# Kernel tuning notes

Hardware: AMD Instinct MI355X
Metric: run time of the kernel (lower is better)

Reference implementation:

```python
import jax, jax.numpy as jnp
import numpy as np


def setup_inputs() -> dict:
    key = jax.random.key(0)
    ks = jax.random.split(key, 9)
    bs, F, T, d_in, Nh, d_out = 4, 8, 256, 64, 8, 64
    std = 2.0  # gaussian_init_delta_std
    return {
        "X": jax.random.normal(ks[0], (bs, F, T, d_in), dtype=jnp.float32),
        "attention_center": std * jax.random.normal(ks[1], (F, Nh, 1), dtype=jnp.float32),
        "alpha": jax.random.normal(ks[2], (F,), dtype=jnp.float32),
        "W_query": jax.random.normal(ks[3], (F, T, d_in, Nh, 2), dtype=jnp.float32),
        "W_key": jax.random.normal(ks[4], (F, T, d_in, Nh, 2), dtype=jnp.float32),
        "Wkey_": jax.random.normal(ks[5], (F, 2, 2), dtype=jnp.float32),
        "u": jax.random.normal(ks[6], (F, T, 2), dtype=jnp.float32),
        "W": jax.random.normal(ks[7], (F, Nh * d_in, d_out), dtype=jnp.float32),
        "b": jax.random.normal(ks[8], (F, T, d_out), dtype=jnp.float32),
    }


def reference(X, attention_center, alpha, W_query, W_key, Wkey_, u, W, b):
    bs, F, T, d_in = X.shape
    Nh = W_query.shape[3]

    # relative-position features R[t,l] = (l-t)^2, (l-t); identical across F in the original
    rel = (jnp.arange(T)[None, :] - jnp.arange(T)[:, None]).astype(jnp.float32)
    R = jnp.stack([rel ** 2, rel], axis=-1)  # (T,T,2)

    query = jnp.einsum('bftd,ftdhe->bfthe', X, W_query)  # (bs,F,T,Nh,2)
    key = jnp.einsum('bftd,ftdhe->bfthe', X, W_key)      # (bs,F,T,Nh,2)

    r_delta = jnp.einsum('fde,tle->ftld', Wkey_, R)      # (F,T,T,2)

    centers = jnp.concatenate([jnp.ones_like(attention_center), -2.0 * attention_center], axis=-1)  # (F,Nh,2)
    v = -alpha[:, None, None] * centers                  # (F,Nh,2)

    scores = (
        jnp.einsum('bfthe,bflhe->bfthl', query, key)
        + jnp.einsum('bfthe,ftle->bfthl', query, r_delta)
        + jnp.einsum('fle,bfthe->bfthl', u, key)
        + jnp.einsum('fhe,ftle->fthl', v, r_delta)[None]
    )  # (bs,F,T,Nh,T)

    probs = jax.nn.softmax(scores, axis=-1)

    vals = jnp.einsum('bfthl,bfld->bfthd', probs, X)     # (bs,F,T,Nh,d_in)
    vals = vals.reshape(bs, F, T, Nh * d_in)

    return jnp.einsum('bftd,fdo->bfto', vals, W) + b     # (bs,F,T,d_out)
```

## Files before the change

### kernel.cpp

```cpp
#include <hip/hip_runtime.h>
#include <hip/hip_bf16.h>

#define BS 4
#define NF 8
#define NT 256
#define DIN 64
#define NH 8
#define DOUT 64
#define TT 8
#define MROWS 64
#define NCHUNK 32

typedef unsigned short u16;
typedef __attribute__((ext_vector_type(8))) short short8;
typedef __attribute__((ext_vector_type(4))) float f32x4;
typedef __attribute__((ext_vector_type(4))) unsigned int u32x4;

static __device__ __forceinline__ u16 f2bf(float x) {
    __hip_bfloat16 h = __float2bfloat16(x);
    u16 r; __builtin_memcpy(&r, &h, 2); return r;
}
static __device__ __forceinline__ unsigned pk2(float a, float b) {
    return (unsigned)f2bf(a) | ((unsigned)f2bf(b) << 16);
}

__global__ __launch_bounds__(256) void prep_kernel(
    const float* __restrict__ X,
    const float* __restrict__ Wq,
    const float* __restrict__ Wk,
    const float* __restrict__ W,
    float* __restrict__ q,
    float* __restrict__ k,
    u16* __restrict__ XT,
    u16* __restrict__ Wt)
{
    __shared__ float sT[64][65];
    const int tid = threadIdx.x;
    const int bid = blockIdx.x;

    if (bid < 1024) {
        const int gw = (bid << 2) + (tid >> 6);
        const int which = gw >> 11;
        const int ft = gw & 2047;
        const int f = ft >> 8, t = ft & 255;
        const int ln = tid & 63;
        const int dg = ln >> 4;
        const int b  = (ln >> 2) & 3;
        const int hq = ln & 3;

        const float* wmat = which ? Wk : Wq;
        const float* wp = wmat + ((size_t)ft << 10) + (dg << 8) + (hq << 2);
        const float* xp = X + (((size_t)((b * NF + f) * NT + t)) << 6) + (dg << 4);

        float4 acc = {0.f, 0.f, 0.f, 0.f};
        #pragma unroll
        for (int j = 0; j < 16; ++j) {
            float xv = xp[j];
            float4 w4 = *(const float4*)(wp + (j << 4));
            acc.x = fmaf(xv, w4.x, acc.x);
            acc.y = fmaf(xv, w4.y, acc.y);
            acc.z = fmaf(xv, w4.z, acc.z);
            acc.w = fmaf(xv, w4.w, acc.w);
        }
        #pragma unroll
        for (int off = 16; off <= 32; off <<= 1) {
            acc.x += __shfl_xor(acc.x, off);
            acc.y += __shfl_xor(acc.y, off);
            acc.z += __shfl_xor(acc.z, off);
            acc.w += __shfl_xor(acc.w, off);
        }
        if (dg == 0) {
            float* outp = which ? k : q;
            *(float4*)(outp + (((size_t)((b * NF + f) * NT + t)) << 4) + (hq << 2)) = acc;
        }
    } else if (bid < 1056) {
        const int bf = bid - 1024;
        for (int lc = 0; lc < 4; ++lc) {
            #pragma unroll
            for (int i = 0; i < 16; ++i) {
                int l = i * 4 + (tid >> 6), d = tid & 63;
                sT[l][d] = X[(((size_t)(bf * NT) + lc * 64 + l) << 6) + d];
            }
            __syncthreads();
            #pragma unroll
            for (int i = 0; i < 16; ++i) {
                int d = i * 4 + (tid >> 6), l = tid & 63;
                XT[(((size_t)(bf * 64) + d) << 8) + lc * 64 + l] = f2bf(sT[l][d]);
            }
            __syncthreads();
        }
    } else {
        const int idx = bid - 1056;
        const int f = idx >> 3, kc = idx & 7;
        #pragma unroll
        for (int i = 0; i < 16; ++i) {
            int kk = i * 4 + (tid >> 6), o = tid & 63;
            sT[kk][o] = W[(((size_t)(f * 512) + kc * 64 + kk) << 6) + o];
        }
        __syncthreads();
        #pragma unroll
        for (int i = 0; i < 16; ++i) {
            int o = i * 4 + (tid >> 6), kk = tid & 63;
            Wt[(((size_t)(f * 64) + o) << 9) + kc * 64 + kk] = f2bf(sT[kk][o]);
        }
    }
}

__global__ __launch_bounds__(256, 3) void attn_kernel(
    const float* __restrict__ ac,
    const float* __restrict__ alpha,
    const float* __restrict__ Wkey_,
    const float* __restrict__ u,
    const float* __restrict__ bias,
    const float* __restrict__ q,
    const float* __restrict__ kws,
    const u16* __restrict__ XT,
    const u16* __restrict__ Wt,
    float* __restrict__ out)
{
    __shared__ u16  sP[MROWS * 256];
    __shared__ float sKU[4608];
    __shared__ float sRed[8 * MROWS];
    __shared__ float sM[MROWS];
    __shared__ float sInvS[MROWS];

    const int tid = threadIdx.x;
    const int bid = blockIdx.x;
    const int ch = bid & 31;
    const int f  = (bid >> 5) & 7;
    const int b  = bid >> 8;
    const int bf = b * NF + f;
    const int t0 = ch * TT;

    {
        const float4* k4 = (const float4*)(kws + ((size_t)bf << 12));
        float4* d4 = (float4*)sKU;
        #pragma unroll
        for (int i = 0; i < 4; ++i) d4[i * 256 + tid] = k4[i * 256 + tid];
        if (tid < 128) ((float4*)(sKU + 4096))[tid] = ((const float4*)(u + f * 512))[tid];
    }
    __syncthreads();

    const int h  = tid & 7;
    const int tp = (tid >> 3) & 3;
    const int le = tid >> 5;
    const int t_a = t0 + tp * 2, t_b = t_a + 1;
    const int m_a = tp * 16 + h, m_b = m_a + 8;
    const int lbase = le * 32;

    float q0a, q1a, kt0a, kt1a, c2a, c1a;
    float q0b, q1b, kt0b, kt1b, c2b, c1b;
    {
        float al = alpha[f];
        float acv = ac[f * 8 + h];
        float wk0 = Wkey_[f * 4],     wk1 = Wkey_[f * 4 + 1];
        float wk2 = Wkey_[f * 4 + 2], wk3 = Wkey_[f * 4 + 3];
        float2 qa = *(const float2*)(q + ((size_t)(bf * NT + t_a) << 4) + (h << 1));
        float2 qb = *(const float2*)(q + ((size_t)(bf * NT + t_b) << 4) + (h << 1));
        q0a = qa.x; q1a = qa.y; q0b = qb.x; q1b = qb.y;
        kt0a = sKU[t_a * 16 + h * 2]; kt1a = sKU[t_a * 16 + h * 2 + 1];
        kt0b = sKU[t_b * 16 + h * 2]; kt1b = sKU[t_b * 16 + h * 2 + 1];
        float a0 = q0a - al, a1 = q1a + 2.f * al * acv;
        c2a = a0 * wk0 + a1 * wk2; c1a = a0 * wk1 + a1 * wk3;
        a0 = q0b - al; a1 = q1b + 2.f * al * acv;
        c2b = a0 * wk0 + a1 * wk2; c1b = a0 * wk1 + a1 * wk3;
    }

    float mxa = -1e30f, mxb = -1e30f;
    {
        float rela = (float)(lbase - t_a);
        #pragma unroll 8
        for (int j = 0; j < 32; ++j) {
            int l = lbase + j;
            float2 K = *(const float2*)(sKU + l * 16 + h * 2);
            float2 U = *(const float2*)(sKU + 4096 + l * 2);
            float relb = rela - 1.f;
            float sa = (c2a * rela + c1a) * rela;
            sa = fmaf(q0a, K.x, sa); sa = fmaf(q1a, K.y, sa);
            sa = fmaf(kt0a, U.x, sa); sa = fmaf(kt1a, U.y, sa);
            float sb = (c2b * relb + c1b) * relb;
            sb = fmaf(q0b, K.x, sb); sb = fmaf(q1b, K.y, sb);
            sb = fmaf(kt0b, U.x, sb); sb = fmaf(kt1b, U.y, sb);
            mxa = fmaxf(mxa, sa); mxb = fmaxf(mxb, sb);
            rela += 1.f;
        }
    }
    sRed[le * 64 + m_a] = mxa;
    sRed[le * 64 + m_b] = mxb;
    __syncthreads();
    if (tid < 64) {
        float mm = sRed[tid];
        #pragma unroll
        for (int i = 1; i < 8; ++i) mm = fmaxf(mm, sRed[i * 64 + tid]);
        sM[tid] = mm;
    }
    __syncthreads();

    {
        const float Ma = sM[m_a], Mb = sM[m_b];
        float suma = 0.f, sumb = 0.f;
        float rela = (float)(lbase - t_a);
        unsigned pka[4], pkb[4];
        float epa = 0.f, epb = 0.f;
        #pragma unroll 8
        for (int j = 0; j < 32; ++j) {
            int l = lbase + j;
            float2 K = *(const float2*)(sKU + l * 16 + h * 2);
            float2 U = *(const float2*)(sKU + 4096 + l * 2);
            float relb = rela - 1.f;
            float sa = (c2a * rela + c1a) * rela;
            sa = fmaf(q0a, K.x, sa); sa = fmaf(q1a, K.y, sa);
            sa = fmaf(kt0a, U.x, sa); sa = fmaf(kt1a, U.y, sa);
            float sb = (c2b * relb + c1b) * relb;
            sb = fmaf(q0b, K.x, sb); sb = fmaf(q1b, K.y, sb);
            sb = fmaf(kt0b, U.x, sb); sb = fmaf(kt1b, U.y, sb);
            float ea = __expf(sa - Ma), eb = __expf(sb - Mb);
            suma += ea; sumb += eb;
            if ((j & 1) == 0) { epa = ea; epb = eb; }
            else { pka[(j & 7) >> 1] = pk2(epa, ea); pkb[(j & 7) >> 1] = pk2(epb, eb); }
            if ((j & 7) == 7) {
                int chunk = l >> 3;
                int pa = chunk ^ (m_a & 15), pb = chunk ^ (m_b & 15);
                *(u32x4*)&sP[m_a * 256 + pa * 8] = (u32x4){pka[0], pka[1], pka[2], pka[3]};
                *(u32x4*)&sP[m_b * 256 + pb * 8] = (u32x4){pkb[0], pkb[1], pkb[2], pkb[3]};
            }
            rela += 1.f;
        }
        sRed[le * 64 + m_a] = suma;
        sRed[le * 64 + m_b] = sumb;
    }

    const int wv   = tid >> 6;
    const int lane = tid & 63;
    const int quad = lane >> 4;
    const int ln   = lane & 15;
    const u16* xb = XT + ((size_t)bf << 14);
    short8 nb0, nb1, nb2, nb3;
    {
        int l = quad * 8;
        nb0 = *(const short8*)(xb + (0 * 16 + ln) * 256 + l);
        nb1 = *(const short8*)(xb + (1 * 16 + ln) * 256 + l);
        nb2 = *(const short8*)(xb + (2 * 16 + ln) * 256 + l);
        nb3 = *(const short8*)(xb + (3 * 16 + ln) * 256 + l);
    }
    __syncthreads();
    if (tid < 64) {
        float ss = sRed[tid];
        #pragma unroll
        for (int i = 1; i < 8; ++i) ss += sRed[i * 64 + tid];
        sInvS[tid] = 1.f / ss;
    }
    __syncthreads();

    f32x4 acc0 = {0.f, 0.f, 0.f, 0.f}, acc1 = acc0, acc2 = acc0, acc3 = acc0;
    #pragma unroll
    for (int ks = 0; ks < 8; ++ks) {
        short8 b0 = nb0, b1 = nb1, b2 = nb2, b3 = nb3;
        if (ks < 7) {
            int l = (ks + 1) * 32 + quad * 8;
            nb0 = *(const short8*)(xb + (0 * 16 + ln) * 256 + l);
            nb1 = *(const short8*)(xb + (1 * 16 + ln) * 256 + l);
            nb2 = *(const short8*)(xb + (2 * 16 + ln) * 256 + l);
            nb3 = *(const short8*)(xb + (3 * 16 + ln) * 256 + l);
        }
        int phys = (ks * 4 + quad) ^ ln;
        short8 a = *(const short8*)&sP[(wv * 16 + ln) * 256 + phys * 8];
        acc0 = __builtin_amdgcn_mfma_f32_16x16x32_bf16(a, b0, acc0, 0, 0, 0);
        acc1 = __builtin_amdgcn_mfma_f32_16x16x32_bf16(a, b1, acc1, 0, 0, 0);
        acc2 = __builtin_amdgcn_mfma_f32_16x16x32_bf16(a, b2, acc2, 0, 0, 0);
        acc3 = __builtin_amdgcn_mfma_f32_16x16x32_bf16(a, b3, acc3, 0, 0, 0);
    }

    u16* sVals = (u16*)sKU;
    #pragma unroll
    for (int reg = 0; reg < 4; ++reg) {
        int mg = wv * 16 + quad * 4 + reg;
        float inv = sInvS[mg];
        int tl = mg >> 3, hh = mg & 7;
        u16* dst = sVals + tl * 520 + hh * 64 + ln;
        dst[0]  = f2bf(acc0[reg] * inv);
        dst[16] = f2bf(acc1[reg] * inv);
        dst[32] = f2bf(acc2[reg] * inv);
        dst[48] = f2bf(acc3[reg] * inv);
    }
    const u16* wb = Wt + ((size_t)(f * 64 + wv * 16 + ln) << 9);
    short8 nw = *(const short8*)(wb + quad * 8);
    __syncthreads();

    f32x4 oacc = {0.f, 0.f, 0.f, 0.f};
    #pragma unroll
    for (int ks = 0; ks < 16; ++ks) {
        short8 bw = nw;
        if (ks < 15) nw = *(const short8*)(wb + (ks + 1) * 32 + quad * 8);
        short8 a = *(const short8*)(sVals + ln * 520 + ks * 32 + quad * 8);
        oacc = __builtin_amdgcn_mfma_f32_16x16x32_bf16(a, bw, oacc, 0, 0, 0);
    }
    {
        int o = wv * 16 + ln;
        #pragma unroll
        for (int reg = 0; reg < 4; ++reg) {
            int tl = quad * 4 + reg;
            if (tl < TT) {
                int tg = t0 + tl;
                out[((size_t)(bf * NT + tg) << 6) + o] =
                    oacc[reg] + bias[((size_t)(f * NT + tg) << 6) + o];
            }
        }
    }
}

extern "C" void kernel_launch(void* const* d_in, const int* in_sizes, int n_in,
                              void* d_out, int out_size, void* d_ws, size_t ws_size,
                              hipStream_t stream) {
    const float* X     = (const float*)d_in[0];
    const float* ac    = (const float*)d_in[1];
    const float* alpha = (const float*)d_in[2];
    const float* Wq    = (const float*)d_in[3];
    const float* Wk    = (const float*)d_in[4];
    const float* Wkey_ = (const float*)d_in[5];
    const float* u     = (const float*)d_in[6];
    const float* W     = (const float*)d_in[7];
    const float* bb    = (const float*)d_in[8];
    float* out = (float*)d_out;

    float* qws = (float*)d_ws;
    float* kws = qws + 131072;
    u16* XT = (u16*)(kws + 131072);
    u16* Wt = XT + 524288;

    hipLaunchKernelGGL(prep_kernel, dim3(1120), dim3(256), 0, stream,
                       X, Wq, Wk, W, qws, kws, XT, Wt);
    hipLaunchKernelGGL(attn_kernel, dim3(BS * NF * NCHUNK), dim3(256), 0, stream,
                       ac, alpha, Wkey_, u, bb, qws, kws, XT, Wt, out);
}
```

Measured before the change: 135.6 us.

## Restructure QK projection reuse and halve attention tile with register-cached scores

The q/k projection now loads each W slice once per wave with coalesced float4 reads. It stages the X rows for all four batches in shared memory and computes all batches from those registers, replacing per-batch strided W reads. The attention kernel halves the rows per block (TT 4), which doubles the grid and raises the occupancy hint. It also keeps the 16 scores per thread in registers so the second pass no longer recomputes them. The PV MFMA work is split across waves along the N dimension, and the reductions use a transposed float4-friendly layout. The risks are more register pressure and more redundant K/U staging per block.

```diff
diff --git a/kernel.cpp b/kernel.cpp
--- a/kernel.cpp
+++ b/kernel.cpp
@@ -7,9 +7,9 @@
 #define DIN 64
 #define NH 8
 #define DOUT 64
-#define TT 8
-#define MROWS 64
-#define NCHUNK 32
+#define TT 4
+#define MROWS 32
+#define NCH 64
 
 typedef unsigned short u16;
 typedef __attribute__((ext_vector_type(8))) short short8;
@@ -35,43 +35,60 @@
     u16* __restrict__ Wt)
 {
     __shared__ float sT[64][65];
+    __shared__ float sXq[4 * 256];
     const int tid = threadIdx.x;
     const int bid = blockIdx.x;
 
     if (bid < 1024) {
-        const int gw = (bid << 2) + (tid >> 6);
+        const int wv = tid >> 6, L = tid & 63;
+        const int gw = (bid << 2) + wv;
         const int which = gw >> 11;
         const int ft = gw & 2047;
         const int f = ft >> 8, t = ft & 255;
-        const int ln = tid & 63;
-        const int dg = ln >> 4;
-        const int b  = (ln >> 2) & 3;
-        const int hq = ln & 3;
 
         const float* wmat = which ? Wk : Wq;
-        const float* wp = wmat + ((size_t)ft << 10) + (dg << 8) + (hq << 2);
-        const float* xp = X + (((size_t)((b * NF + f) * NT + t)) << 6) + (dg << 4);
-
-        float4 acc = {0.f, 0.f, 0.f, 0.f};
-        #pragma unroll
-        for (int j = 0; j < 16; ++j) {
-            float xv = xp[j];
-            float4 w4 = *(const float4*)(wp + (j << 4));
-            acc.x = fmaf(xv, w4.x, acc.x);
-            acc.y = fmaf(xv, w4.y, acc.y);
-            acc.z = fmaf(xv, w4.z, acc.z);
-            acc.w = fmaf(xv, w4.w, acc.w);
-        }
-        #pragma unroll
-        for (int off = 16; off <= 32; off <<= 1) {
-            acc.x += __shfl_xor(acc.x, off);
-            acc.y += __shfl_xor(acc.y, off);
-            acc.z += __shfl_xor(acc.z, off);
-            acc.w += __shfl_xor(acc.w, off);
-        }
-        if (dg == 0) {
+        const float* wp = wmat + ((size_t)ft << 10);
+        float4 w0 = *(const float4*)(wp + (L << 2));
+        float4 w1 = *(const float4*)(wp + 256 + (L << 2));
+        float4 w2 = *(const float4*)(wp + 512 + (L << 2));
+        float4 w3 = *(const float4*)(wp + 768 + (L << 2));
+
+        float* sx = sXq + (wv << 8);
+        {
+            int xb = L >> 4, d4 = (L & 15) << 2;
+            *(float4*)(sx + (xb << 6) + d4) =
+                *(const float4*)(X + (((size_t)((xb * NF + f) * NT + t)) << 6) + d4);
+        }
+        const int dr = L >> 2;
+        float4 acc[4];
+        #pragma unroll
+        for (int bb = 0; bb < 4; ++bb) {
+            float x0 = sx[(bb << 6) + dr];
+            float x1 = sx[(bb << 6) + 16 + dr];
+            float x2 = sx[(bb << 6) + 32 + dr];
+            float x3 = sx[(bb << 6) + 48 + dr];
+            float4 a;
+            a.x = fmaf(x0, w0.x, fmaf(x1, w1.x, fmaf(x2, w2.x, x3 * w3.x)));
+            a.y = fmaf(x0, w0.y, fmaf(x1, w1.y, fmaf(x2, w2.y, x3 * w3.y)));
+            a.z = fmaf(x0, w0.z, fmaf(x1, w1.z, fmaf(x2, w2.z, x3 * w3.z)));
+            a.w = fmaf(x0, w0.w, fmaf(x1, w1.w, fmaf(x2, w2.w, x3 * w3.w)));
+            acc[bb] = a;
+        }
+        #pragma unroll
+        for (int off = 4; off <= 32; off <<= 1) {
+            #pragma unroll
+            for (int bb = 0; bb < 4; ++bb) {
+                acc[bb].x += __shfl_xor(acc[bb].x, off);
+                acc[bb].y += __shfl_xor(acc[bb].y, off);
+                acc[bb].z += __shfl_xor(acc[bb].z, off);
+                acc[bb].w += __shfl_xor(acc[bb].w, off);
+            }
+        }
+        if (L < 4) {
             float* outp = which ? k : q;
-            *(float4*)(outp + (((size_t)((b * NF + f) * NT + t)) << 4) + (hq << 2)) = acc;
+            #pragma unroll
+            for (int bb = 0; bb < 4; ++bb)
+                *(float4*)(outp + (((size_t)((bb * NF + f) * NT + t)) << 4) + (L << 2)) = acc[bb];
         }
     } else if (bid < 1056) {
         const int bf = bid - 1024;
@@ -106,7 +123,7 @@
     }
 }
 
-__global__ __launch_bounds__(256, 3) void attn_kernel(
+__global__ __launch_bounds__(256, 4) void attn_kernel(
     const float* __restrict__ ac,
     const float* __restrict__ alpha,
     const float* __restrict__ Wkey_,
@@ -120,15 +137,15 @@
 {
     __shared__ u16  sP[MROWS * 256];
     __shared__ float sKU[4608];
-    __shared__ float sRed[8 * MROWS];
+    __shared__ float sRed[MROWS * 16];
     __shared__ float sM[MROWS];
     __shared__ float sInvS[MROWS];
 
     const int tid = threadIdx.x;
     const int bid = blockIdx.x;
-    const int ch = bid & 31;
-    const int f  = (bid >> 5) & 7;
-    const int b  = bid >> 8;
+    const int ch = bid & 63;
+    const int f  = (bid >> 6) & 7;
+    const int b  = bid >> 9;
     const int bf = b * NF + f;
     const int t0 = ch * TT;
 
@@ -142,11 +159,11 @@
     __syncthreads();
 
     const int h  = tid & 7;
-    const int tp = (tid >> 3) & 3;
-    const int le = tid >> 5;
+    const int tp = (tid >> 3) & 1;
+    const int lg = tid >> 4;
     const int t_a = t0 + tp * 2, t_b = t_a + 1;
     const int m_a = tp * 16 + h, m_b = m_a + 8;
-    const int lbase = le * 32;
+    const int lbase = lg * 16;
 
     float q0a, q1a, kt0a, kt1a, c2a, c1a;
     float q0b, q1b, kt0b, kt1b, c2b, c1b;
@@ -166,11 +183,12 @@
         c2b = a0 * wk0 + a1 * wk2; c1b = a0 * wk1 + a1 * wk3;
     }
 
+    float sA[16], sB[16];
     float mxa = -1e30f, mxb = -1e30f;
     {
         float rela = (float)(lbase - t_a);
-        #pragma unroll 8
-        for (int j = 0; j < 32; ++j) {
+        #pragma unroll
+        for (int j = 0; j < 16; ++j) {
             int l = lbase + j;
             float2 K = *(const float2*)(sKU + l * 16 + h * 2);
             float2 U = *(const float2*)(sKU + 4096 + l * 2);
@@ -181,17 +199,21 @@
             float sb = (c2b * relb + c1b) * relb;
             sb = fmaf(q0b, K.x, sb); sb = fmaf(q1b, K.y, sb);
             sb = fmaf(kt0b, U.x, sb); sb = fmaf(kt1b, U.y, sb);
+            sA[j] = sa; sB[j] = sb;
             mxa = fmaxf(mxa, sa); mxb = fmaxf(mxb, sb);
             rela += 1.f;
         }
     }
-    sRed[le * 64 + m_a] = mxa;
-    sRed[le * 64 + m_b] = mxb;
-    __syncthreads();
-    if (tid < 64) {
-        float mm = sRed[tid];
-        #pragma unroll
-        for (int i = 1; i < 8; ++i) mm = fmaxf(mm, sRed[i * 64 + tid]);
+    sRed[m_a * 16 + lg] = mxa;
+    sRed[m_b * 16 + lg] = mxb;
+    __syncthreads();
+    if (tid < MROWS) {
+        const float4* r4 = (const float4*)(sRed + tid * 16);
+        float4 r0 = r4[0], r1 = r4[1], r2 = r4[2], r3 = r4[3];
+        float mm = fmaxf(fmaxf(fmaxf(r0.x, r0.y), fmaxf(r0.z, r0.w)),
+                         fmaxf(fmaxf(r1.x, r1.y), fmaxf(r1.z, r1.w)));
+        mm = fmaxf(mm, fmaxf(fmaxf(fmaxf(r2.x, r2.y), fmaxf(r2.z, r2.w)),
+                             fmaxf(fmaxf(r3.x, r3.y), fmaxf(r3.z, r3.w))));
         sM[tid] = mm;
     }
     __syncthreads();
@@ -199,89 +221,73 @@
     {
         const float Ma = sM[m_a], Mb = sM[m_b];
         float suma = 0.f, sumb = 0.f;
-        float rela = (float)(lbase - t_a);
         unsigned pka[4], pkb[4];
         float epa = 0.f, epb = 0.f;
-        #pragma unroll 8
-        for (int j = 0; j < 32; ++j) {
-            int l = lbase + j;
-            float2 K = *(const float2*)(sKU + l * 16 + h * 2);
-            float2 U = *(const float2*)(sKU + 4096 + l * 2);
-            float relb = rela - 1.f;
-            float sa = (c2a * rela + c1a) * rela;
-            sa = fmaf(q0a, K.x, sa); sa = fmaf(q1a, K.y, sa);
-            sa = fmaf(kt0a, U.x, sa); sa = fmaf(kt1a, U.y, sa);
-            float sb = (c2b * relb + c1b) * relb;
-            sb = fmaf(q0b, K.x, sb); sb = fmaf(q1b, K.y, sb);
-            sb = fmaf(kt0b, U.x, sb); sb = fmaf(kt1b, U.y, sb);
-            float ea = __expf(sa - Ma), eb = __expf(sb - Mb);
+        #pragma unroll
+        for (int j = 0; j < 16; ++j) {
+            float ea = __expf(sA[j] - Ma), eb = __expf(sB[j] - Mb);
             suma += ea; sumb += eb;
             if ((j & 1) == 0) { epa = ea; epb = eb; }
             else { pka[(j & 7) >> 1] = pk2(epa, ea); pkb[(j & 7) >> 1] = pk2(epb, eb); }
             if ((j & 7) == 7) {
-                int chunk = l >> 3;
-                int pa = chunk ^ (m_a & 15), pb = chunk ^ (m_b & 15);
+                int chunk = lg * 2 + (j >> 3);
+                int pa = chunk ^ h;
+                int pb = chunk ^ (h + 8);
                 *(u32x4*)&sP[m_a * 256 + pa * 8] = (u32x4){pka[0], pka[1], pka[2], pka[3]};
                 *(u32x4*)&sP[m_b * 256 + pb * 8] = (u32x4){pkb[0], pkb[1], pkb[2], pkb[3]};
             }
-            rela += 1.f;
-        }
-        sRed[le * 64 + m_a] = suma;
-        sRed[le * 64 + m_b] = sumb;
+        }
+        sRed[m_a * 16 + lg] = suma;
+        sRed[m_b * 16 + lg] = sumb;
     }
 
     const int wv   = tid >> 6;
     const int lane = tid & 63;
     const int quad = lane >> 4;
     const int ln   = lane & 15;
+    const int mh   = wv & 1;
+    const int nh   = wv >> 1;
     const u16* xb = XT + ((size_t)bf << 14);
-    short8 nb0, nb1, nb2, nb3;
-    {
-        int l = quad * 8;
-        nb0 = *(const short8*)(xb + (0 * 16 + ln) * 256 + l);
-        nb1 = *(const short8*)(xb + (1 * 16 + ln) * 256 + l);
-        nb2 = *(const short8*)(xb + (2 * 16 + ln) * 256 + l);
-        nb3 = *(const short8*)(xb + (3 * 16 + ln) * 256 + l);
-    }
-    __syncthreads();
-    if (tid < 64) {
-        float ss = sRed[tid];
-        #pragma unroll
-        for (int i = 1; i < 8; ++i) ss += sRed[i * 64 + tid];
+    short8 nb0, nb1;
+    {
+        int l2 = quad * 8;
+        nb0 = *(const short8*)(xb + (nh * 32 + ln) * 256 + l2);
+        nb1 = *(const short8*)(xb + (nh * 32 + 16 + ln) * 256 + l2);
+    }
+    __syncthreads();
+    if (tid < MROWS) {
+        const float4* r4 = (const float4*)(sRed + tid * 16);
+        float4 r0 = r4[0], r1 = r4[1], r2 = r4[2], r3 = r4[3];
+        float ss = ((r0.x + r0.y) + (r0.z + r0.w)) + ((r1.x + r1.y) + (r1.z + r1.w))
+                 + ((r2.x + r2.y) + (r2.z + r2.w)) + ((r3.x + r3.y) + (r3.z + r3.w));
         sInvS[tid] = 1.f / ss;
     }
     __syncthreads();
 
-    f32x4 acc0 = {0.f, 0.f, 0.f, 0.f}, acc1 = acc0, acc2 = acc0, acc3 = acc0;
+    f32x4 acc0 = {0.f, 0.f, 0.f, 0.f}, acc1 = acc0;
     #pragma unroll
     for (int ks = 0; ks < 8; ++ks) {
-        short8 b0 = nb0, b1 = nb1, b2 = nb2, b3 = nb3;
+        short8 b0 = nb0, b1 = nb1;
         if (ks < 7) {
-            int l = (ks + 1) * 32 + quad * 8;
-            nb0 = *(const short8*)(xb + (0 * 16 + ln) * 256 + l);
-            nb1 = *(const short8*)(xb + (1 * 16 + ln) * 256 + l);
-            nb2 = *(const short8*)(xb + (2 * 16 + ln) * 256 + l);
-            nb3 = *(const short8*)(xb + (3 * 16 + ln) * 256 + l);
+            int l2 = (ks + 1) * 32 + quad * 8;
+            nb0 = *(const short8*)(xb + (nh * 32 + ln) * 256 + l2);
+            nb1 = *(const short8*)(xb + (nh * 32 + 16 + ln) * 256 + l2);
         }
         int phys = (ks * 4 + quad) ^ ln;
-        short8 a = *(const short8*)&sP[(wv * 16 + ln) * 256 + phys * 8];
+        short8 a = *(const short8*)&sP[(mh * 16 + ln) * 256 + phys * 8];
         acc0 = __builtin_amdgcn_mfma_f32_16x16x32_bf16(a, b0, acc0, 0, 0, 0);
         acc1 = __builtin_amdgcn_mfma_f32_16x16x32_bf16(a, b1, acc1, 0, 0, 0);
-        acc2 = __builtin_amdgcn_mfma_f32_16x16x32_bf16(a, b2, acc2, 0, 0, 0);
-        acc3 = __builtin_amdgcn_mfma_f32_16x16x32_bf16(a, b3, acc3, 0, 0, 0);
     }
 
     u16* sVals = (u16*)sKU;
     #pragma unroll
     for (int reg = 0; reg < 4; ++reg) {
-        int mg = wv * 16 + quad * 4 + reg;
+        int mg = mh * 16 + quad * 4 + reg;
         float inv = sInvS[mg];
         int tl = mg >> 3, hh = mg & 7;
-        u16* dst = sVals + tl * 520 + hh * 64 + ln;
+        u16* dst = sVals + tl * 520 + hh * 64 + nh * 32 + ln;
         dst[0]  = f2bf(acc0[reg] * inv);
         dst[16] = f2bf(acc1[reg] * inv);
-        dst[32] = f2bf(acc2[reg] * inv);
-        dst[48] = f2bf(acc3[reg] * inv);
     }
     const u16* wb = Wt + ((size_t)(f * 64 + wv * 16 + ln) << 9);
     short8 nw = *(const short8*)(wb + quad * 8);
@@ -330,6 +336,6 @@
 
     hipLaunchKernelGGL(prep_kernel, dim3(1120), dim3(256), 0, stream,
                        X, Wq, Wk, W, qws, kws, XT, Wt);
-    hipLaunchKernelGGL(attn_kernel, dim3(BS * NF * NCHUNK), dim3(256), 0, stream,
+    hipLaunchKernelGGL(attn_kernel, dim3(BS * NF * NCH), dim3(256), 0, stream,
                        ac, alpha, Wkey_, u, bb, qws, kws, XT, Wt, out);
 }
```

After: 119.0 us. -12.3%, faster.
